# Performance work log

Measured on AMD Instinct MI355X. Metric: run time of the kernel, lower is better.

Reference implementation:

```python
import jax, jax.numpy as jnp
import numpy as np

N, H, W, D = 4, 32, 32, 64
NH = 8
L = 4             # num_layers
DFF = 4 * D       # dim_feedforward
PRUNE_RATIO = 0.3
LN_EPS = 1e-5


def setup_inputs() -> dict:
    key = jax.random.key(0)
    ks = jax.random.split(key, 10)
    rn = lambda k, shape: (jax.random.normal(k, shape, dtype=jnp.float32) * 0.02)
    n_keep = int(D * PRUNE_RATIO)
    prune_mask = jnp.concatenate([jnp.ones((n_keep,), jnp.float32), jnp.zeros((D - n_keep,), jnp.float32)])
    return {
        "hsi_features": jax.random.normal(ks[0], (N, H, W, D), dtype=jnp.float32),
        "rgb_features": jax.random.normal(ks[1], (N, H, W, D), dtype=jnp.float32),
        "in_proj_w": rn(ks[2], (L, 3 * D, D)),
        "in_proj_b": jnp.zeros((L, 3 * D), jnp.float32),
        "out_w": rn(ks[3], (L, D, D)),
        "out_b": jnp.zeros((L, D), jnp.float32),
        "lin1_w": rn(ks[4], (L, DFF, D)),
        "lin1_b": jnp.zeros((L, DFF), jnp.float32),
        "lin2_w": rn(ks[5], (L, D, DFF)),
        "lin2_b": jnp.zeros((L, D), jnp.float32),
        "ln1_w": jnp.ones((L, D), jnp.float32),
        "ln1_b": jnp.zeros((L, D), jnp.float32),
        "ln2_w": jnp.ones((L, D), jnp.float32),
        "ln2_b": jnp.zeros((L, D), jnp.float32),
        "prune_mask": prune_mask,
    }


def _ln(x, w, b):
    mu = x.mean(-1, keepdims=True)
    var = ((x - mu) ** 2).mean(-1, keepdims=True)
    return (x - mu) * jax.lax.rsqrt(var + LN_EPS) * w + b


def _encoder_layer(x, p):
    # Post-LN TransformerEncoderLayer (torch default, eval mode -> no dropout).
    in_w, in_b, ow, ob, l1w, l1b, l2w, l2b, n1w, n1b, n2w, n2b = p
    M = x.shape[0]
    hd = D // NH
    qkv = x @ in_w.T + in_b                       # [M, 3D]
    q, k, v = jnp.split(qkv, 3, axis=-1)
    q = q.reshape(M, NH, hd).transpose(1, 0, 2)   # [NH, M, hd]
    k = k.reshape(M, NH, hd).transpose(1, 0, 2)
    v = v.reshape(M, NH, hd).transpose(1, 0, 2)
    scale = 1.0 / jnp.sqrt(jnp.float32(hd))
    att = jax.nn.softmax(jnp.einsum('hmd,hnd->hmn', q * scale, k), axis=-1)  # [NH, M, M]
    o = jnp.einsum('hmn,hnd->hmd', att, v).transpose(1, 0, 2).reshape(M, D)
    o = o @ ow.T + ob
    x = _ln(x + o, n1w, n1b)
    ff = jax.nn.relu(x @ l1w.T + l1b) @ l2w.T + l2b
    return _ln(x + ff, n2w, n2b)


def _mmd(x, y, sigma=1.0):
    # Gaussian-kernel MMD; ||a-b||^2 via norms + GEMM (no MxMxD intermediate).
    def gk_mean(a, b):
        d = (a * a).sum(-1)[:, None] + (b * b).sum(-1)[None, :] - 2.0 * (a @ b.T)
        return jnp.exp(-d / (2.0 * sigma ** 2)).mean()
    return gk_mean(x, x) + gk_mean(y, y) - 2.0 * gk_mean(x, y)


def _forward(hsi_features, rgb_features, in_proj_w, in_proj_b, out_w, out_b,
             lin1_w, lin1_b, lin2_w, lin2_b, ln1_w, ln1_b, ln2_w, ln2_b, prune_mask):
    Nb, Hh, Ww, C = hsi_features.shape
    x = hsi_features.reshape(-1, C)               # [M, D], M = N*H*W tokens (batch=1)
    for i in range(L):
        x = _encoder_layer(x, (in_proj_w[i], in_proj_b[i], out_w[i], out_b[i],
                               lin1_w[i], lin1_b[i], lin2_w[i], lin2_b[i],
                               ln1_w[i], ln1_b[i], ln2_w[i], ln2_b[i]))
    x = x * prune_mask
    mmd_loss = _mmd(x, rgb_features.reshape(-1, C))
    return x.reshape(Nb, Hh, Ww, C), mmd_loss


def reference(hsi_features, rgb_features, in_proj_w, in_proj_b, out_w, out_b,
              lin1_w, lin1_b, lin2_w, lin2_b, ln1_w, ln1_b, ln2_w, ln2_b, prune_mask):
    return _forward(hsi_features, rgb_features, in_proj_w, in_proj_b, out_w, out_b,
                    lin1_w, lin1_b, lin2_w, lin2_b, ln1_w, ln1_b, ln2_w, ln2_b, prune_mask)
```

## Files before the change

### kernel.cpp

```cpp
#include <hip/hip_runtime.h>

#define MT 4096
#define DM 64
#define NHEAD 8
#define HDIM 8
#define DFF 256
#define NLAYER 4
#define LN_EPS 1e-5f

#define QSCALE 0.51011784f
#define MMDC (-0.72134752f)

#if __has_builtin(__builtin_amdgcn_exp2f)
#define EXP2(x) __builtin_amdgcn_exp2f(x)
#else
#define EXP2(x) exp2f(x)
#endif

typedef __attribute__((ext_vector_type(8))) short bf16x8;
typedef __attribute__((ext_vector_type(4))) short bf16x4;
typedef __attribute__((ext_vector_type(4))) float f32x4;

__device__ __forceinline__ float wave_sum64(float v) {
#pragma unroll
  for (int m = 1; m < 64; m <<= 1) v += __shfl_xor(v, m, 64);
  return v;
}

__device__ __forceinline__ short f2bf(float x) {
  union { float f; unsigned u; } v; v.f = x;
  unsigned r = v.u + 0x7fffu + ((v.u >> 16) & 1u);
  return (short)(r >> 16);
}

__device__ __forceinline__ unsigned packbf2(float a, float b) {
  union { float f; unsigned u; } x, y; x.f = a; y.f = b;
  return __builtin_amdgcn_perm(y.u, x.u, 0x07060302u);
}

__global__ void prep_kernel(const float* __restrict__ inw, float* __restrict__ Wti,
                            const float* __restrict__ ow,  float* __restrict__ Wto,
                            const float* __restrict__ l1w, float* __restrict__ Wt1,
                            const float* __restrict__ l2w, float* __restrict__ Wt2,
                            const float* __restrict__ rgb, short* __restrict__ rgbb,
                            float* __restrict__ nrm) {
  const int bid = blockIdx.x;
  const int tid = threadIdx.x;
  if (bid >= 192) {
    const int row = (bid - 192) * 4 + (tid >> 6);
    const int d = tid & 63;
    float v = rgb[(size_t)row * DM + d];
    rgbb[(size_t)row * DM + d] = f2bf(v);
    float s = wave_sum64(v * v);
    if (d == 0) nrm[MT + row] = s;
    return;
  }
  const float* src; float* dst; int R, C, r0, c0;
  if (bid < 48) {
    int l = bid / 12, t = bid % 12;
    src = inw + (size_t)l * 12288; dst = Wti + (size_t)l * 12288;
    R = 192; C = 64; c0 = (t % 2) * 32; r0 = (t / 2) * 32;
  } else if (bid < 64) {
    int idx = bid - 48, l = idx / 4, t = idx % 4;
    src = ow + (size_t)l * 4096; dst = Wto + (size_t)l * 4096;
    R = 64; C = 64; c0 = (t % 2) * 32; r0 = (t / 2) * 32;
  } else if (bid < 128) {
    int idx = bid - 64, l = idx / 16, t = idx % 16;
    src = l1w + (size_t)l * 16384; dst = Wt1 + (size_t)l * 16384;
    R = 256; C = 64; c0 = (t % 2) * 32; r0 = (t / 2) * 32;
  } else {
    int idx = bid - 128, l = idx / 16, t = idx % 16;
    src = l2w + (size_t)l * 16384; dst = Wt2 + (size_t)l * 16384;
    R = 64; C = 256; c0 = (t % 8) * 32; r0 = (t / 8) * 32;
  }
  __shared__ float tl[32][33];
  const int tx = tid & 31, ty = tid >> 5;
  for (int rr = ty; rr < 32; rr += 8)
    tl[rr][tx] = src[(size_t)(r0 + rr) * C + c0 + tx];
  __syncthreads();
  for (int idx = tid; idx < 1024; idx += 256) {
    const int k4l = idx >> 7, rem = idx & 127, ol = rem >> 2, j = rem & 3;
    dst[(((size_t)(c0 >> 2) + k4l) * R + r0 + ol) * 4 + j] = tl[ol][k4l * 4 + j];
  }
}

__global__ __launch_bounds__(192) void qkv0_kernel(const float* __restrict__ hsi,
                                                   const float* __restrict__ Wt,
                                                   const float* __restrict__ B,
                                                   float* __restrict__ x,
                                                   short* __restrict__ Qbf,
                                                   short* __restrict__ Kbf,
                                                   short* __restrict__ Vtb) {
  const int t0 = blockIdx.x * 4;
  const int o = threadIdx.x;
  __shared__ float xr[4][DM];
  for (int e = o; e < 64; e += 192) {
    float4 v = ((const float4*)(hsi + (size_t)t0 * DM))[e];
    ((float4*)xr)[e] = v;
    ((float4*)(x + (size_t)t0 * DM))[e] = v;
  }
  __syncthreads();
  float acc0 = B[o], acc1 = acc0, acc2 = acc0, acc3 = acc0;
#pragma unroll 8
  for (int k4 = 0; k4 < 16; ++k4) {
    float4 w4 = ((const float4*)Wt)[k4 * 192 + o];
    float4 a = *(const float4*)&xr[0][k4 * 4];
    acc0 += a.x * w4.x + a.y * w4.y + a.z * w4.z + a.w * w4.w;
    float4 b = *(const float4*)&xr[1][k4 * 4];
    acc1 += b.x * w4.x + b.y * w4.y + b.z * w4.z + b.w * w4.w;
    float4 c = *(const float4*)&xr[2][k4 * 4];
    acc2 += c.x * w4.x + c.y * w4.y + c.z * w4.z + c.w * w4.w;
    float4 d = *(const float4*)&xr[3][k4 * 4];
    acc3 += d.x * w4.x + d.y * w4.y + d.z * w4.z + d.w * w4.w;
  }
  if (o < 128) {
    const int c = o & 63, hh = c >> 3, ch = c & 7;
    short* dst = (o < 64) ? Qbf : Kbf;
    const float sc = (o < 64) ? QSCALE : 1.0f;
    dst[((size_t)hh * MT + t0 + 0) * 8 + ch] = f2bf(acc0 * sc);
    dst[((size_t)hh * MT + t0 + 1) * 8 + ch] = f2bf(acc1 * sc);
    dst[((size_t)hh * MT + t0 + 2) * 8 + ch] = f2bf(acc2 * sc);
    dst[((size_t)hh * MT + t0 + 3) * 8 + ch] = f2bf(acc3 * sc);
  } else {
    const int c = o - 128;
    bf16x4 v = {f2bf(acc0), f2bf(acc1), f2bf(acc2), f2bf(acc3)};
    *(bf16x4*)&Vtb[(size_t)c * MT + t0] = v;
  }
}

__global__ __launch_bounds__(256, 8) void attn_kernel(const short* __restrict__ Qbf,
                                                      const short* __restrict__ Kbf,
                                                      const short* __restrict__ Vtb,
                                                      float* __restrict__ pbuf,
                                                      float* __restrict__ lbuf) {
  const int h = blockIdx.y;
  const int qbase = blockIdx.x * 64;
  const int z = blockIdx.z;
  const int tid = threadIdx.x;
  const int wid = tid >> 6;
  const int lane = tid & 63;
  const int n = lane & 15;
  const int quad = lane >> 4;

  __shared__ short Klds[2][128 * 8];
  __shared__ short Vtlds[2][9 * 136];
  __shared__ short Plds[4][16 * 72];

  if (tid < 32) {
    bf16x8 ones = {0x3F80, 0x3F80, 0x3F80, 0x3F80, 0x3F80, 0x3F80, 0x3F80, 0x3F80};
    *(bf16x8*)&Vtlds[tid >> 4][8 * 136 + (tid & 15) * 8] = ones;
  }

  const bf16x8 zero8 = {0, 0, 0, 0, 0, 0, 0, 0};
  bf16x8 qb = zero8;
  if (quad == 0) qb = *(const bf16x8*)&Qbf[((size_t)h * MT + qbase + wid * 16 + n) * 8];

  {
    const int k0 = z * 1024;
    if (tid < 128) {
      *(bf16x8*)&Klds[0][tid * 8] = *(const bf16x8*)&Kbf[((size_t)h * MT + k0 + tid) * 8];
    } else {
      const int t2 = tid - 128, ch = t2 >> 4, seg = t2 & 15;
      *(bf16x8*)&Vtlds[0][ch * 136 + seg * 8] =
          *(const bf16x8*)&Vtb[((size_t)h * 8 + ch) * MT + k0 + seg * 8];
    }
  }
  __syncthreads();

  f32x4 o_acc = {0.f, 0.f, 0.f, 0.f};

  for (int kt = 0; kt < 8; ++kt) {
    const int buf = kt & 1;
    if (kt < 7) {
      const int k1 = z * 1024 + (kt + 1) * 128;
      if (tid < 128) {
        *(bf16x8*)&Klds[buf ^ 1][tid * 8] = *(const bf16x8*)&Kbf[((size_t)h * MT + k1 + tid) * 8];
      } else {
        const int t2 = tid - 128, ch = t2 >> 4, seg = t2 & 15;
        *(bf16x8*)&Vtlds[buf ^ 1][ch * 136 + seg * 8] =
            *(const bf16x8*)&Vtb[((size_t)h * 8 + ch) * MT + k1 + seg * 8];
      }
    }

#pragma unroll
    for (int sub = 0; sub < 2; ++sub) {
      const short* kbase = &Klds[buf][sub * 64 * 8];
      f32x4 s[4];
#pragma unroll
      for (int mt = 0; mt < 4; ++mt) {
        bf16x8 ka = zero8;
        if (quad == 0) ka = *(const bf16x8*)&kbase[(mt * 16 + n) * 8];
        f32x4 zf = {0.f, 0.f, 0.f, 0.f};
        s[mt] = __builtin_amdgcn_mfma_f32_16x16x32_bf16(ka, qb, zf, 0, 0, 0);
      }

      short* pw = &Plds[wid][n * 72 + quad * 4];
#pragma unroll
      for (int mt = 0; mt < 4; ++mt) {
        unsigned lo = packbf2(EXP2(s[mt][0]), EXP2(s[mt][1]));
        unsigned hi = packbf2(EXP2(s[mt][2]), EXP2(s[mt][3]));
        uint2 pv = {lo, hi};
        *(uint2*)(pw + mt * 16) = pv;
      }

#pragma unroll
      for (int c = 0; c < 2; ++c) {
        bf16x8 va = zero8;
        if (n < 9) va = *(const bf16x8*)&Vtlds[buf][n * 136 + sub * 64 + c * 32 + quad * 8];
        bf16x8 pb = *(const bf16x8*)&Plds[wid][n * 72 + c * 32 + quad * 8];
        o_acc = __builtin_amdgcn_mfma_f32_16x16x32_bf16(va, pb, o_acc, 0, 0, 0);
      }
    }
    __syncthreads();
  }

  const int tok = qbase + wid * 16 + n;
  if (quad < 2) {
    float4 val = {o_acc[0], o_acc[1], o_acc[2], o_acc[3]};
    *(float4*)&pbuf[((size_t)z * MT + tok) * DM + h * 8 + quad * 4] = val;
  }
  if (quad == 2) lbuf[(size_t)z * MT * 8 + (size_t)tok * 8 + h] = o_acc[0];
}

__global__ __launch_bounds__(256) void dense_kernel(
    const float* __restrict__ pbuf, const float* __restrict__ lbuf,
    float* __restrict__ x,
    const float* __restrict__ Wto, const float* __restrict__ ob,
    const float* __restrict__ n1w, const float* __restrict__ n1b,
    const float* __restrict__ Wt1, const float* __restrict__ b1,
    const float* __restrict__ Wt2, const float* __restrict__ b2,
    const float* __restrict__ n2w, const float* __restrict__ n2b,
    const float* __restrict__ Wti, const float* __restrict__ inb,
    short* __restrict__ Qbf, short* __restrict__ Kbf, short* __restrict__ Vtb,
    int do_qkv,
    const float* __restrict__ mask, float* __restrict__ out,
    short* __restrict__ xmb, float* __restrict__ nrm, int do_final) {
  const int t0 = blockIdx.x * 8;
  const int tid = threadIdx.x;
  const int w = tid >> 6, d = tid & 63;

  __shared__ float orow[8][DM];
  __shared__ float x1[8][DM];
  __shared__ float fr[8][DFF];
  __shared__ float x2s[8][DM];

#pragma unroll
  for (int tt = 0; tt < 2; ++tt) {
    const int t = w + tt * 4, tok = t0 + t, h = d >> 3;
    float o = 0.f, l = 0.f;
#pragma unroll
    for (int z = 0; z < 4; ++z) {
      o += pbuf[((size_t)z * MT + tok) * DM + d];
      l += lbuf[(size_t)z * MT * 8 + (size_t)tok * 8 + h];
    }
    orow[t][d] = o / l;
  }
  __syncthreads();

  {
    float acc[2] = {ob[d], ob[d]};
#pragma unroll 8
    for (int k4 = 0; k4 < 16; ++k4) {
      float4 w4 = ((const float4*)Wto)[k4 * 64 + d];
      float4 a = *(const float4*)&orow[w][k4 * 4];
      acc[0] += a.x * w4.x + a.y * w4.y + a.z * w4.z + a.w * w4.w;
      float4 b = *(const float4*)&orow[w + 4][k4 * 4];
      acc[1] += b.x * w4.x + b.y * w4.y + b.z * w4.z + b.w * w4.w;
    }
#pragma unroll
    for (int tt = 0; tt < 2; ++tt) {
      const int t = w + tt * 4, tok = t0 + t;
      float hv = x[(size_t)tok * DM + d] + acc[tt];
      float mu = wave_sum64(hv) * (1.0f / DM);
      float dv = hv - mu;
      float var = wave_sum64(dv * dv) * (1.0f / DM);
      x1[t][d] = dv * rsqrtf(var + LN_EPS) * n1w[d] + n1b[d];
    }
  }
  __syncthreads();

  {
    const int o = tid;
    float acc[8];
#pragma unroll
    for (int t = 0; t < 8; ++t) acc[t] = b1[o];
#pragma unroll 8
    for (int k4 = 0; k4 < 16; ++k4) {
      float4 w4 = ((const float4*)Wt1)[k4 * 256 + o];
#pragma unroll
      for (int t = 0; t < 8; ++t) {
        float4 a = *(const float4*)&x1[t][k4 * 4];
        acc[t] += a.x * w4.x + a.y * w4.y + a.z * w4.z + a.w * w4.w;
      }
    }
#pragma unroll
    for (int t = 0; t < 8; ++t) fr[t][o] = fmaxf(acc[t], 0.0f);
  }
  __syncthreads();

  {
    float acc[2] = {b2[d], b2[d]};
#pragma unroll 8
    for (int k4 = 0; k4 < 64; ++k4) {
      float4 w4 = ((const float4*)Wt2)[k4 * 64 + d];
      float4 a = *(const float4*)&fr[w][k4 * 4];
      acc[0] += a.x * w4.x + a.y * w4.y + a.z * w4.z + a.w * w4.w;
      float4 b = *(const float4*)&fr[w + 4][k4 * 4];
      acc[1] += b.x * w4.x + b.y * w4.y + b.z * w4.z + b.w * w4.w;
    }
#pragma unroll
    for (int tt = 0; tt < 2; ++tt) {
      const int t = w + tt * 4, tok = t0 + t;
      float hv = x1[t][d] + acc[tt];
      float mu = wave_sum64(hv) * (1.0f / DM);
      float dv = hv - mu;
      float var = wave_sum64(dv * dv) * (1.0f / DM);
      float v = dv * rsqrtf(var + LN_EPS) * n2w[d] + n2b[d];
      x2s[t][d] = v;
      x[(size_t)tok * DM + d] = v;
      if (do_final) {
        float pv = v * mask[d];
        out[(size_t)tok * DM + d] = pv;
        xmb[(size_t)tok * DM + d] = f2bf(pv);
        float s = wave_sum64(pv * pv);
        if (d == 0) nrm[tok] = s;
      }
    }
  }
  __syncthreads();

  if (do_qkv && tid < 192) {
    const int o = tid;
    float acc[8];
#pragma unroll
    for (int t = 0; t < 8; ++t) acc[t] = inb[o];
#pragma unroll 8
    for (int k4 = 0; k4 < 16; ++k4) {
      float4 w4 = ((const float4*)Wti)[k4 * 192 + o];
#pragma unroll
      for (int t = 0; t < 8; ++t) {
        float4 a = *(const float4*)&x2s[t][k4 * 4];
        acc[t] += a.x * w4.x + a.y * w4.y + a.z * w4.z + a.w * w4.w;
      }
    }
    if (o < 128) {
      const int c = o & 63, hh = c >> 3, ch = c & 7;
      short* dst = (o < 64) ? Qbf : Kbf;
      const float sc = (o < 64) ? QSCALE : 1.0f;
#pragma unroll
      for (int t = 0; t < 8; ++t)
        dst[((size_t)hh * MT + t0 + t) * 8 + ch] = f2bf(acc[t] * sc);
    } else {
      bf16x8 v = {f2bf(acc[0]), f2bf(acc[1]), f2bf(acc[2]), f2bf(acc[3]),
                  f2bf(acc[4]), f2bf(acc[5]), f2bf(acc[6]), f2bf(acc[7])};
      *(bf16x8*)&Vtb[(size_t)(o - 128) * MT + t0] = v;
    }
  }
}

__global__ __launch_bounds__(256) void mmd_kernel(const short* __restrict__ xmb,
                                                  const short* __restrict__ rgbb,
                                                  const float* __restrict__ nrm,
                                                  float* __restrict__ partials) {
  const int bid = blockIdx.x;
  int p, bx, by;
  float coef;
  if (bid < 1024) {
    p = 2; bx = bid & 31; by = bid >> 5; coef = -2.0f;
  } else {
    const int t = bid - 1024;
    p = (t < 528) ? 0 : 1;
    const int u = (t < 528) ? t : t - 528;
    by = (int)((sqrtf(8.0f * (float)u + 1.0f) - 1.0f) * 0.5f);
    while ((by + 1) * (by + 2) / 2 <= u) ++by;
    while (by * (by + 1) / 2 > u) --by;
    bx = u - by * (by + 1) / 2;
    coef = (bx == by) ? 1.0f : 2.0f;
  }
  const short* A = (p == 1) ? rgbb : xmb;
  const short* B = (p == 0) ? xmb : rgbb;
  const float* nA = (p == 1) ? (nrm + MT) : nrm;
  const float* nB = (p == 0) ? nrm : (nrm + MT);
  const int i0 = bx * 128;
  const int j0 = by * 128;
  const int tid = threadIdx.x;
  const int wid = tid >> 6;
  const int lane = tid & 63;
  const int n = lane & 15;
  const int quad = lane >> 4;

  bf16x8 a0[2], a1[2];
  float na[2][4];
#pragma unroll
  for (int s = 0; s < 2; ++s) {
    const int arow = i0 + wid * 32 + s * 16 + n;
    a0[s] = *(const bf16x8*)&A[(size_t)arow * DM + quad * 8];
    a1[s] = *(const bf16x8*)&A[(size_t)arow * DM + 32 + quad * 8];
#pragma unroll
    for (int r = 0; r < 4; ++r) na[s][r] = nA[i0 + wid * 32 + s * 16 + quad * 4 + r];
  }
  bf16x8 b0[8], b1[8];
  float nb[8];
#pragma unroll
  for (int nt = 0; nt < 8; ++nt) {
    const int brow = j0 + nt * 16 + n;
    b0[nt] = *(const bf16x8*)&B[(size_t)brow * DM + quad * 8];
    b1[nt] = *(const bf16x8*)&B[(size_t)brow * DM + 32 + quad * 8];
    nb[nt] = nB[j0 + nt * 16 + n];
  }

  float local = 0.f;
#pragma unroll
  for (int nt = 0; nt < 8; ++nt) {
#pragma unroll
    for (int s = 0; s < 2; ++s) {
      f32x4 zf = {0.f, 0.f, 0.f, 0.f};
      f32x4 d4 = __builtin_amdgcn_mfma_f32_16x16x32_bf16(a0[s], b0[nt], zf, 0, 0, 0);
      d4 = __builtin_amdgcn_mfma_f32_16x16x32_bf16(a1[s], b1[nt], d4, 0, 0, 0);
#pragma unroll
      for (int r = 0; r < 4; ++r) {
        float dist = na[s][r] + nb[nt] - 2.0f * d4[r];
        local += EXP2(MMDC * dist);
      }
    }
  }

  float tot = wave_sum64(local);
  __shared__ float wpart[4];
  if (lane == 0) wpart[wid] = tot;
  __syncthreads();
  if (tid == 0)
    partials[bid] = coef * (wpart[0] + wpart[1] + wpart[2] + wpart[3]);
}

__global__ __launch_bounds__(256) void reducefin_kernel(const float* __restrict__ partials,
                                                        float* __restrict__ out) {
  const int tid = threadIdx.x;
  float s = 0.f;
  for (int i = tid; i < 2080; i += 256) s += partials[i];
  s = wave_sum64(s);
  __shared__ float L[4];
  if ((tid & 63) == 0) L[tid >> 6] = s;
  __syncthreads();
  if (tid == 0) {
    const float invn = 1.0f / ((float)MT * (float)MT);
    out[(size_t)MT * DM] = (L[0] + L[1] + L[2] + L[3]) * invn;
  }
}

extern "C" void kernel_launch(void* const* d_in, const int* in_sizes, int n_in,
                              void* d_out, int out_size, void* d_ws, size_t ws_size,
                              hipStream_t stream) {
  const float* hsi  = (const float*)d_in[0];
  const float* rgb  = (const float*)d_in[1];
  const float* inw  = (const float*)d_in[2];
  const float* inb  = (const float*)d_in[3];
  const float* ow   = (const float*)d_in[4];
  const float* obv  = (const float*)d_in[5];
  const float* l1w  = (const float*)d_in[6];
  const float* l1b  = (const float*)d_in[7];
  const float* l2w  = (const float*)d_in[8];
  const float* l2b  = (const float*)d_in[9];
  const float* n1w  = (const float*)d_in[10];
  const float* n1b  = (const float*)d_in[11];
  const float* n2w  = (const float*)d_in[12];
  const float* n2b  = (const float*)d_in[13];
  const float* mask = (const float*)d_in[14];
  float* out = (float*)d_out;

  float* ws     = (float*)d_ws;
  float* x      = ws;
  float* pbuf   = ws + 262144;
  float* lbuf   = ws + 1310720;
  float* nrm    = ws + 1441792;
  float* parts  = ws + 1449984;
  float* Wti    = ws + 1454080;
  float* Wto    = ws + 1503232;
  float* Wt1    = ws + 1519616;
  float* Wt2    = ws + 1585152;
  short* xmb    = (short*)(ws + 1650688);
  short* rgbb   = (short*)(ws + 1781760);
  short* Qbf    = (short*)(ws + 1912832);
  short* Kbf    = (short*)(ws + 2043904);
  short* Vtb    = (short*)(ws + 2174976);

  prep_kernel<<<192 + MT / 4, 256, 0, stream>>>(inw, Wti, ow, Wto, l1w, Wt1, l2w, Wt2,
                                                rgb, rgbb, nrm);
  qkv0_kernel<<<MT / 4, 192, 0, stream>>>(hsi, Wti, inb, x, Qbf, Kbf, Vtb);

  for (int i = 0; i < NLAYER; ++i) {
    attn_kernel<<<dim3(MT / 64, NHEAD, 4), 256, 0, stream>>>(Qbf, Kbf, Vtb, pbuf, lbuf);
    const int last = (i == NLAYER - 1);
    dense_kernel<<<MT / 8, 256, 0, stream>>>(
        pbuf, lbuf, x,
        Wto + (size_t)i * DM * DM, obv + (size_t)i * DM,
        n1w + (size_t)i * DM, n1b + (size_t)i * DM,
        Wt1 + (size_t)i * DFF * DM, l1b + (size_t)i * DFF,
        Wt2 + (size_t)i * DM * DFF, l2b + (size_t)i * DM,
        n2w + (size_t)i * DM, n2b + (size_t)i * DM,
        Wti + (size_t)(last ? 0 : (i + 1)) * 192 * DM,
        inb + (size_t)(last ? 0 : (i + 1)) * 192,
        Qbf, Kbf, Vtb, !last,
        mask, out, xmb, nrm, last);
  }

  mmd_kernel<<<2080, 256, 0, stream>>>(xmb, rgbb, nrm, parts);
  reducefin_kernel<<<1, 256, 0, stream>>>(parts, out);
}
```

Before: 315.9 us.

## Use 32x32x8 f16 MFMA for QK scores, split keys eightway, fuse qkv0 into prep

Q and K are stored as fp16 so attention can compute scores with the 32x32x8 f16 MFMA. This avoids the old 16x16x32 bf16 path, where three quarters of the operand lanes were zero padding because the head dim is only 8. Each block now handles 128 queries, and the key range is split eight ways instead of four, which doubles the pbuf/lbuf partial traffic the dense kernel must reduce. The separate layer-0 QKV kernel is merged into prep_kernel, reading the untransposed weights directly, which removes one launch. fp16 Q/K changes the rounding behaviour relative to bf16.

```diff
diff --git a/kernel.cpp b/kernel.cpp
--- a/kernel.cpp
+++ b/kernel.cpp
@@ -7,6 +7,7 @@
 #define DFF 256
 #define NLAYER 4
 #define LN_EPS 1e-5f
+#define ZSPLIT 8
 
 #define QSCALE 0.51011784f
 #define MMDC (-0.72134752f)
@@ -20,6 +21,8 @@
 typedef __attribute__((ext_vector_type(8))) short bf16x8;
 typedef __attribute__((ext_vector_type(4))) short bf16x4;
 typedef __attribute__((ext_vector_type(4))) float f32x4;
+typedef __attribute__((ext_vector_type(16))) float f32x16;
+typedef __attribute__((ext_vector_type(4))) _Float16 f16x4;
 
 __device__ __forceinline__ float wave_sum64(float v) {
 #pragma unroll
@@ -38,14 +41,57 @@
   return __builtin_amdgcn_perm(y.u, x.u, 0x07060302u);
 }
 
-__global__ void prep_kernel(const float* __restrict__ inw, float* __restrict__ Wti,
-                            const float* __restrict__ ow,  float* __restrict__ Wto,
-                            const float* __restrict__ l1w, float* __restrict__ Wt1,
-                            const float* __restrict__ l2w, float* __restrict__ Wt2,
-                            const float* __restrict__ rgb, short* __restrict__ rgbb,
-                            float* __restrict__ nrm) {
+__global__ __launch_bounds__(256) void prep_kernel(
+    const float* __restrict__ inw, float* __restrict__ Wti,
+    const float* __restrict__ ow,  float* __restrict__ Wto,
+    const float* __restrict__ l1w, float* __restrict__ Wt1,
+    const float* __restrict__ l2w, float* __restrict__ Wt2,
+    const float* __restrict__ rgb, short* __restrict__ rgbb, float* __restrict__ nrm,
+    const float* __restrict__ hsi, const float* __restrict__ inb, float* __restrict__ x,
+    _Float16* __restrict__ Qh, _Float16* __restrict__ Kh, short* __restrict__ Vtb) {
   const int bid = blockIdx.x;
   const int tid = threadIdx.x;
+  if (bid >= 1216) {
+    const int t0 = (bid - 1216) * 4;
+    __shared__ float xr[4][DM];
+    if (tid < 64) {
+      float4 v = ((const float4*)(hsi + (size_t)t0 * DM))[tid];
+      ((float4*)xr)[tid] = v;
+      ((float4*)(x + (size_t)t0 * DM))[tid] = v;
+    }
+    __syncthreads();
+    const int o = tid;
+    if (o < 192) {
+      float acc0 = inb[o], acc1 = acc0, acc2 = acc0, acc3 = acc0;
+      const float* wrow = inw + (size_t)o * DM;
+#pragma unroll 8
+      for (int k4 = 0; k4 < 16; ++k4) {
+        float4 w4 = *(const float4*)&wrow[k4 * 4];
+        float4 a = *(const float4*)&xr[0][k4 * 4];
+        acc0 += a.x * w4.x + a.y * w4.y + a.z * w4.z + a.w * w4.w;
+        float4 b = *(const float4*)&xr[1][k4 * 4];
+        acc1 += b.x * w4.x + b.y * w4.y + b.z * w4.z + b.w * w4.w;
+        float4 c = *(const float4*)&xr[2][k4 * 4];
+        acc2 += c.x * w4.x + c.y * w4.y + c.z * w4.z + c.w * w4.w;
+        float4 d = *(const float4*)&xr[3][k4 * 4];
+        acc3 += d.x * w4.x + d.y * w4.y + d.z * w4.z + d.w * w4.w;
+      }
+      if (o < 128) {
+        const int c = o & 63, hh = c >> 3, ch = c & 7;
+        _Float16* dst = (o < 64) ? Qh : Kh;
+        const float sc = (o < 64) ? QSCALE : 1.0f;
+        dst[((size_t)hh * MT + t0 + 0) * 8 + ch] = (_Float16)(acc0 * sc);
+        dst[((size_t)hh * MT + t0 + 1) * 8 + ch] = (_Float16)(acc1 * sc);
+        dst[((size_t)hh * MT + t0 + 2) * 8 + ch] = (_Float16)(acc2 * sc);
+        dst[((size_t)hh * MT + t0 + 3) * 8 + ch] = (_Float16)(acc3 * sc);
+      } else {
+        const int c = o - 128;
+        bf16x4 v = {f2bf(acc0), f2bf(acc1), f2bf(acc2), f2bf(acc3)};
+        *(bf16x4*)&Vtb[(size_t)c * MT + t0] = v;
+      }
+    }
+    return;
+  }
   if (bid >= 192) {
     const int row = (bid - 192) * 4 + (tid >> 6);
     const int d = tid & 63;
@@ -84,81 +130,38 @@
   }
 }
 
-__global__ __launch_bounds__(192) void qkv0_kernel(const float* __restrict__ hsi,
-                                                   const float* __restrict__ Wt,
-                                                   const float* __restrict__ B,
-                                                   float* __restrict__ x,
-                                                   short* __restrict__ Qbf,
-                                                   short* __restrict__ Kbf,
-                                                   short* __restrict__ Vtb) {
-  const int t0 = blockIdx.x * 4;
-  const int o = threadIdx.x;
-  __shared__ float xr[4][DM];
-  for (int e = o; e < 64; e += 192) {
-    float4 v = ((const float4*)(hsi + (size_t)t0 * DM))[e];
-    ((float4*)xr)[e] = v;
-    ((float4*)(x + (size_t)t0 * DM))[e] = v;
-  }
-  __syncthreads();
-  float acc0 = B[o], acc1 = acc0, acc2 = acc0, acc3 = acc0;
-#pragma unroll 8
-  for (int k4 = 0; k4 < 16; ++k4) {
-    float4 w4 = ((const float4*)Wt)[k4 * 192 + o];
-    float4 a = *(const float4*)&xr[0][k4 * 4];
-    acc0 += a.x * w4.x + a.y * w4.y + a.z * w4.z + a.w * w4.w;
-    float4 b = *(const float4*)&xr[1][k4 * 4];
-    acc1 += b.x * w4.x + b.y * w4.y + b.z * w4.z + b.w * w4.w;
-    float4 c = *(const float4*)&xr[2][k4 * 4];
-    acc2 += c.x * w4.x + c.y * w4.y + c.z * w4.z + c.w * w4.w;
-    float4 d = *(const float4*)&xr[3][k4 * 4];
-    acc3 += d.x * w4.x + d.y * w4.y + d.z * w4.z + d.w * w4.w;
-  }
-  if (o < 128) {
-    const int c = o & 63, hh = c >> 3, ch = c & 7;
-    short* dst = (o < 64) ? Qbf : Kbf;
-    const float sc = (o < 64) ? QSCALE : 1.0f;
-    dst[((size_t)hh * MT + t0 + 0) * 8 + ch] = f2bf(acc0 * sc);
-    dst[((size_t)hh * MT + t0 + 1) * 8 + ch] = f2bf(acc1 * sc);
-    dst[((size_t)hh * MT + t0 + 2) * 8 + ch] = f2bf(acc2 * sc);
-    dst[((size_t)hh * MT + t0 + 3) * 8 + ch] = f2bf(acc3 * sc);
-  } else {
-    const int c = o - 128;
-    bf16x4 v = {f2bf(acc0), f2bf(acc1), f2bf(acc2), f2bf(acc3)};
-    *(bf16x4*)&Vtb[(size_t)c * MT + t0] = v;
-  }
-}
-
-__global__ __launch_bounds__(256, 8) void attn_kernel(const short* __restrict__ Qbf,
-                                                      const short* __restrict__ Kbf,
+__global__ __launch_bounds__(256, 6) void attn_kernel(const _Float16* __restrict__ Qh,
+                                                      const _Float16* __restrict__ Kh,
                                                       const short* __restrict__ Vtb,
                                                       float* __restrict__ pbuf,
                                                       float* __restrict__ lbuf) {
   const int h = blockIdx.y;
-  const int qbase = blockIdx.x * 64;
+  const int qbase = blockIdx.x * 128;
   const int z = blockIdx.z;
   const int tid = threadIdx.x;
   const int wid = tid >> 6;
   const int lane = tid & 63;
+  const int l31 = lane & 31;
+  const int hi = lane >> 5;
   const int n = lane & 15;
   const int quad = lane >> 4;
 
   __shared__ short Klds[2][128 * 8];
   __shared__ short Vtlds[2][9 * 136];
-  __shared__ short Plds[4][16 * 72];
+  __shared__ short Plds[4][32 * 72];
 
   if (tid < 32) {
     bf16x8 ones = {0x3F80, 0x3F80, 0x3F80, 0x3F80, 0x3F80, 0x3F80, 0x3F80, 0x3F80};
     *(bf16x8*)&Vtlds[tid >> 4][8 * 136 + (tid & 15) * 8] = ones;
   }
 
+  const f16x4 qb = *(const f16x4*)&Qh[((size_t)h * MT + qbase + wid * 32 + l31) * 8 + hi * 4];
   const bf16x8 zero8 = {0, 0, 0, 0, 0, 0, 0, 0};
-  bf16x8 qb = zero8;
-  if (quad == 0) qb = *(const bf16x8*)&Qbf[((size_t)h * MT + qbase + wid * 16 + n) * 8];
 
   {
-    const int k0 = z * 1024;
+    const int k0 = z * 512;
     if (tid < 128) {
-      *(bf16x8*)&Klds[0][tid * 8] = *(const bf16x8*)&Kbf[((size_t)h * MT + k0 + tid) * 8];
+      *(bf16x8*)&Klds[0][tid * 8] = *(const bf16x8*)&Kh[((size_t)h * MT + k0 + tid) * 8];
     } else {
       const int t2 = tid - 128, ch = t2 >> 4, seg = t2 & 15;
       *(bf16x8*)&Vtlds[0][ch * 136 + seg * 8] =
@@ -167,14 +170,15 @@
   }
   __syncthreads();
 
-  f32x4 o_acc = {0.f, 0.f, 0.f, 0.f};
-
-  for (int kt = 0; kt < 8; ++kt) {
+  f32x4 o_acc0 = {0.f, 0.f, 0.f, 0.f};
+  f32x4 o_acc1 = {0.f, 0.f, 0.f, 0.f};
+
+  for (int kt = 0; kt < 4; ++kt) {
     const int buf = kt & 1;
-    if (kt < 7) {
-      const int k1 = z * 1024 + (kt + 1) * 128;
+    if (kt < 3) {
+      const int k1 = z * 512 + (kt + 1) * 128;
       if (tid < 128) {
-        *(bf16x8*)&Klds[buf ^ 1][tid * 8] = *(const bf16x8*)&Kbf[((size_t)h * MT + k1 + tid) * 8];
+        *(bf16x8*)&Klds[buf ^ 1][tid * 8] = *(const bf16x8*)&Kh[((size_t)h * MT + k1 + tid) * 8];
       } else {
         const int t2 = tid - 128, ch = t2 >> 4, seg = t2 & 15;
         *(bf16x8*)&Vtlds[buf ^ 1][ch * 136 + seg * 8] =
@@ -183,43 +187,40 @@
     }
 
 #pragma unroll
-    for (int sub = 0; sub < 2; ++sub) {
-      const short* kbase = &Klds[buf][sub * 64 * 8];
-      f32x4 s[4];
-#pragma unroll
-      for (int mt = 0; mt < 4; ++mt) {
-        bf16x8 ka = zero8;
-        if (quad == 0) ka = *(const bf16x8*)&kbase[(mt * 16 + n) * 8];
-        f32x4 zf = {0.f, 0.f, 0.f, 0.f};
-        s[mt] = __builtin_amdgcn_mfma_f32_16x16x32_bf16(ka, qb, zf, 0, 0, 0);
-      }
-
-      short* pw = &Plds[wid][n * 72 + quad * 4];
-#pragma unroll
-      for (int mt = 0; mt < 4; ++mt) {
-        unsigned lo = packbf2(EXP2(s[mt][0]), EXP2(s[mt][1]));
-        unsigned hi = packbf2(EXP2(s[mt][2]), EXP2(s[mt][3]));
-        uint2 pv = {lo, hi};
-        *(uint2*)(pw + mt * 16) = pv;
-      }
-
-#pragma unroll
-      for (int c = 0; c < 2; ++c) {
-        bf16x8 va = zero8;
-        if (n < 9) va = *(const bf16x8*)&Vtlds[buf][n * 136 + sub * 64 + c * 32 + quad * 8];
-        bf16x8 pb = *(const bf16x8*)&Plds[wid][n * 72 + c * 32 + quad * 8];
-        o_acc = __builtin_amdgcn_mfma_f32_16x16x32_bf16(va, pb, o_acc, 0, 0, 0);
-      }
+    for (int c32 = 0; c32 < 4; ++c32) {
+      f16x4 ka = *(const f16x4*)&((const _Float16*)Klds[buf])[(c32 * 32 + l31) * 8 + hi * 4];
+      f32x16 zf = {0.f, 0.f, 0.f, 0.f, 0.f, 0.f, 0.f, 0.f,
+                   0.f, 0.f, 0.f, 0.f, 0.f, 0.f, 0.f, 0.f};
+      f32x16 s = __builtin_amdgcn_mfma_f32_32x32x8f16(ka, qb, zf, 0, 0, 0);
+      short* pw = &Plds[wid][l31 * 72 + c32 * 32 + 4 * hi];
+#pragma unroll
+      for (int rg = 0; rg < 4; ++rg) {
+        unsigned lo = packbf2(EXP2(s[4 * rg + 0]), EXP2(s[4 * rg + 1]));
+        unsigned hi2 = packbf2(EXP2(s[4 * rg + 2]), EXP2(s[4 * rg + 3]));
+        uint2 pv = {lo, hi2};
+        *(uint2*)(pw + rg * 8) = pv;
+      }
+      bf16x8 va = zero8;
+      if (n < 9) va = *(const bf16x8*)&Vtlds[buf][n * 136 + c32 * 32 + quad * 8];
+      bf16x8 p0 = *(const bf16x8*)&Plds[wid][n * 72 + c32 * 32 + quad * 8];
+      o_acc0 = __builtin_amdgcn_mfma_f32_16x16x32_bf16(va, p0, o_acc0, 0, 0, 0);
+      bf16x8 p1 = *(const bf16x8*)&Plds[wid][(n + 16) * 72 + c32 * 32 + quad * 8];
+      o_acc1 = __builtin_amdgcn_mfma_f32_16x16x32_bf16(va, p1, o_acc1, 0, 0, 0);
     }
     __syncthreads();
   }
 
-  const int tok = qbase + wid * 16 + n;
+  const int tok0 = qbase + wid * 32 + n;
   if (quad < 2) {
-    float4 val = {o_acc[0], o_acc[1], o_acc[2], o_acc[3]};
-    *(float4*)&pbuf[((size_t)z * MT + tok) * DM + h * 8 + quad * 4] = val;
-  }
-  if (quad == 2) lbuf[(size_t)z * MT * 8 + (size_t)tok * 8 + h] = o_acc[0];
+    float4 v0 = {o_acc0[0], o_acc0[1], o_acc0[2], o_acc0[3]};
+    *(float4*)&pbuf[((size_t)z * MT + tok0) * DM + h * 8 + quad * 4] = v0;
+    float4 v1 = {o_acc1[0], o_acc1[1], o_acc1[2], o_acc1[3]};
+    *(float4*)&pbuf[((size_t)z * MT + tok0 + 16) * DM + h * 8 + quad * 4] = v1;
+  }
+  if (quad == 2) {
+    lbuf[(size_t)z * MT * 8 + (size_t)tok0 * 8 + h] = o_acc0[0];
+    lbuf[(size_t)z * MT * 8 + (size_t)(tok0 + 16) * 8 + h] = o_acc1[0];
+  }
 }
 
 __global__ __launch_bounds__(256) void dense_kernel(
@@ -231,7 +232,7 @@
     const float* __restrict__ Wt2, const float* __restrict__ b2,
     const float* __restrict__ n2w, const float* __restrict__ n2b,
     const float* __restrict__ Wti, const float* __restrict__ inb,
-    short* __restrict__ Qbf, short* __restrict__ Kbf, short* __restrict__ Vtb,
+    _Float16* __restrict__ Qh, _Float16* __restrict__ Kh, short* __restrict__ Vtb,
     int do_qkv,
     const float* __restrict__ mask, float* __restrict__ out,
     short* __restrict__ xmb, float* __restrict__ nrm, int do_final) {
@@ -249,7 +250,7 @@
     const int t = w + tt * 4, tok = t0 + t, h = d >> 3;
     float o = 0.f, l = 0.f;
 #pragma unroll
-    for (int z = 0; z < 4; ++z) {
+    for (int z = 0; z < ZSPLIT; ++z) {
       o += pbuf[((size_t)z * MT + tok) * DM + d];
       l += lbuf[(size_t)z * MT * 8 + (size_t)tok * 8 + h];
     }
@@ -345,11 +346,11 @@
     }
     if (o < 128) {
       const int c = o & 63, hh = c >> 3, ch = c & 7;
-      short* dst = (o < 64) ? Qbf : Kbf;
+      _Float16* dst = (o < 64) ? Qh : Kh;
       const float sc = (o < 64) ? QSCALE : 1.0f;
 #pragma unroll
       for (int t = 0; t < 8; ++t)
-        dst[((size_t)hh * MT + t0 + t) * 8 + ch] = f2bf(acc[t] * sc);
+        dst[((size_t)hh * MT + t0 + t) * 8 + ch] = (_Float16)(acc[t] * sc);
     } else {
       bf16x8 v = {f2bf(acc[0]), f2bf(acc[1]), f2bf(acc[2]), f2bf(acc[3]),
                   f2bf(acc[4]), f2bf(acc[5]), f2bf(acc[6]), f2bf(acc[7])};
@@ -468,28 +469,28 @@
   const float* mask = (const float*)d_in[14];
   float* out = (float*)d_out;
 
-  float* ws     = (float*)d_ws;
-  float* x      = ws;
-  float* pbuf   = ws + 262144;
-  float* lbuf   = ws + 1310720;
-  float* nrm    = ws + 1441792;
-  float* parts  = ws + 1449984;
-  float* Wti    = ws + 1454080;
-  float* Wto    = ws + 1503232;
-  float* Wt1    = ws + 1519616;
-  float* Wt2    = ws + 1585152;
-  short* xmb    = (short*)(ws + 1650688);
-  short* rgbb   = (short*)(ws + 1781760);
-  short* Qbf    = (short*)(ws + 1912832);
-  short* Kbf    = (short*)(ws + 2043904);
-  short* Vtb    = (short*)(ws + 2174976);
-
-  prep_kernel<<<192 + MT / 4, 256, 0, stream>>>(inw, Wti, ow, Wto, l1w, Wt1, l2w, Wt2,
-                                                rgb, rgbb, nrm);
-  qkv0_kernel<<<MT / 4, 192, 0, stream>>>(hsi, Wti, inb, x, Qbf, Kbf, Vtb);
+  float* ws      = (float*)d_ws;
+  float* x       = ws;
+  float* pbuf    = ws + 262144;
+  float* lbuf    = ws + 2359296;
+  float* nrm     = ws + 2621440;
+  float* parts   = ws + 2629632;
+  float* Wti     = ws + 2633728;
+  float* Wto     = ws + 2682880;
+  float* Wt1     = ws + 2699264;
+  float* Wt2     = ws + 2764800;
+  short* xmb     = (short*)(ws + 2830336);
+  short* rgbb    = (short*)(ws + 2961408);
+  _Float16* Qh   = (_Float16*)(ws + 3092480);
+  _Float16* Kh   = (_Float16*)(ws + 3223552);
+  short* Vtb     = (short*)(ws + 3354624);
+
+  prep_kernel<<<192 + MT / 4 + MT / 4, 256, 0, stream>>>(
+      inw, Wti, ow, Wto, l1w, Wt1, l2w, Wt2, rgb, rgbb, nrm,
+      hsi, inb, x, Qh, Kh, Vtb);
 
   for (int i = 0; i < NLAYER; ++i) {
-    attn_kernel<<<dim3(MT / 64, NHEAD, 4), 256, 0, stream>>>(Qbf, Kbf, Vtb, pbuf, lbuf);
+    attn_kernel<<<dim3(MT / 128, NHEAD, ZSPLIT), 256, 0, stream>>>(Qh, Kh, Vtb, pbuf, lbuf);
     const int last = (i == NLAYER - 1);
     dense_kernel<<<MT / 8, 256, 0, stream>>>(
         pbuf, lbuf, x,
@@ -500,7 +501,7 @@
         n2w + (size_t)i * DM, n2b + (size_t)i * DM,
         Wti + (size_t)(last ? 0 : (i + 1)) * 192 * DM,
         inb + (size_t)(last ? 0 : (i + 1)) * 192,
-        Qbf, Kbf, Vtb, !last,
+        Qh, Kh, Vtb, !last,
         mask, out, xmb, nrm, last);
   }
 
```

After: 311.9 us. Within noise of the previous version (-1.3%).
